# Kernel tuning notes

Hardware: AMD Instinct MI355X
Metric: run time of the kernel (lower is better)

Reference implementation:

```python
import jax, jax.numpy as jnp
import numpy as np

B, S, D, H = 8, 512, 1024, 8
DPH = D // H            # 128, dim per head
MAX_REL = 32
NGRAM = 2               # 2-gram RNN on heads 4..7
NG_START, NG_COUNT = 4, 4
SCALE = float(DPH) ** 0.5


def setup_inputs() -> dict:
    key = jax.random.key(0)
    ks = jax.random.split(key, 12)
    w = lambda k, shp: jax.random.normal(k, shp, jnp.float32) * 0.02
    return {
        "x": jax.random.normal(ks[0], (B, S, D), jnp.float32),
        "mask": jax.random.randint(ks[1], (B, 1, S), 0, 2).astype(bool),
        "Wq": w(ks[2], (D, D)), "bq": jnp.zeros((D,), jnp.float32),
        "Wk": w(ks[3], (D, D)), "bk": jnp.zeros((D,), jnp.float32),
        "Wv": w(ks[4], (D, D)), "bv": jnp.zeros((D,), jnp.float32),
        "Wo": w(ks[5], (D, D)), "bo": jnp.zeros((D,), jnp.float32),
        "rel_emb": w(ks[6], (2 * MAX_REL + 1, DPH)),
        "Wih_f": w(ks[7], (DPH, DPH)), "Whh_f": w(ks[8], (DPH, DPH)),
        "bih_f": jnp.zeros((DPH,), jnp.float32), "bhh_f": jnp.zeros((DPH,), jnp.float32),
        "Wih_b": w(ks[9], (DPH, DPH)), "Whh_b": w(ks[10], (DPH, DPH)),
        "bih_b": jnp.zeros((DPH,), jnp.float32), "bhh_b": jnp.zeros((DPH,), jnp.float32),
    }


def reference(x, mask, Wq, bq, Wk, bk, Wv, bv, Wo, bo, rel_emb,
              Wih_f, Whh_f, bih_f, bhh_f, Wih_b, Whh_b, bih_b, bhh_b):
    shape_h = lambda t: t.reshape(B, S, H, DPH).transpose(0, 2, 1, 3)  # [B,H,S,d]
    q = shape_h(x @ Wq.T + bq)
    k = shape_h(x @ Wk.T + bk)
    v = shape_h(x @ Wv.T + bv)

    # --- ngram path: zero masked positions in q/k/v (all heads) ---
    m = mask[:, :, :, None]  # [B,1,S,1] broadcast over heads and d
    q = jnp.where(m, 0.0, q)
    k = jnp.where(m, 0.0, k)
    v = jnp.where(m, 0.0, v)

    # per-head 2-gram bidirectional RNN on heads NG_START..NG_START+NG_COUNT-1
    qh = q[:, NG_START:NG_START + NG_COUNT].reshape(-1, S, DPH)
    kh = k[:, NG_START:NG_START + NG_COUNT].reshape(-1, S, DPH)
    vh = v[:, NG_START:NG_START + NG_COUNT].reshape(-1, S, DPH)
    feats = jnp.concatenate([qh, kh, vh], axis=0)          # [3*B*NG_COUNT, S, d]
    shifted = jnp.pad(feats, ((0, 0), (1, 0), (0, 0)))[:, :-1]  # shift-by-1 (prev token)
    seq = jnp.stack([shifted, feats], axis=0).reshape(NGRAM, -1, DPH)  # [T, N*S, d]
    h0 = jnp.zeros((seq.shape[1], DPH), jnp.float32)
    fstep = lambda h, xt: (jnp.tanh(xt @ Wih_f.T + bih_f + h @ Whh_f.T + bhh_f), None)
    bstep = lambda h, xt: (jnp.tanh(xt @ Wih_b.T + bih_b + h @ Whh_b.T + bhh_b), None)
    hf, _ = jax.lax.scan(fstep, h0, seq)            # fwd final hidden
    hb, _ = jax.lax.scan(bstep, h0, seq[::-1])      # bwd final hidden
    yy = (hf + hb).reshape(3, B, NG_COUNT, S, DPH)  # sum of direction finals
    q = q.at[:, NG_START:NG_START + NG_COUNT].set(yy[0])
    k = k.at[:, NG_START:NG_START + NG_COUNT].set(yy[1])
    v = v.at[:, NG_START:NG_START + NG_COUNT].set(yy[2])

    # --- relative-position attention ---
    qs = q / SCALE
    r = jnp.arange(S)
    rel_idx = jnp.clip(r[None, :] - r[:, None], -MAX_REL, MAX_REL) + MAX_REL  # [S,S]
    rel_k = rel_emb[rel_idx]  # [S,S,d]; same table used for keys and values
    scores = jnp.einsum('bhqd,bhkd->bhqk', qs, k) + jnp.einsum('bhqd,qkd->bhqk', qs, rel_k)
    scores = jnp.where(mask[:, None], -1e18, scores)  # [B,1,1,S] broadcast
    attn = jax.nn.softmax(scores, axis=-1)
    ctx = jnp.einsum('bhqk,bhkd->bhqd', attn, v) + jnp.einsum('bhqk,qkd->bhqd', attn, rel_k)
    out = ctx.transpose(0, 2, 1, 3).reshape(B, S, D) @ Wo.T + bo
    return out, attn
```

## Files before the change

### kernel.cpp

```cpp
#include <hip/hip_runtime.h>


typedef __bf16 bf16x8 __attribute__((ext_vector_type(8)));
typedef float f32x4 __attribute__((ext_vector_type(4)));

#define MFMA16(a, b, c) __builtin_amdgcn_mfma_f32_16x16x32_bf16(a, b, c, 0, 0, 0)

__device__ __forceinline__ unsigned short f2bf(float f) {
  unsigned u = __float_as_uint(f);
  u += 0x7FFFu + ((u >> 16) & 1u);
  return (unsigned short)(u >> 16);
}
__device__ __forceinline__ uint2 pack4(float4 f) {
  uint2 r;
  r.x = (unsigned)f2bf(f.x) | ((unsigned)f2bf(f.y) << 16);
  r.y = (unsigned)f2bf(f.z) | ((unsigned)f2bf(f.w) << 16);
  return r;
}
__device__ __forceinline__ void gld16(const unsigned short* g, unsigned short* l) {
  __builtin_amdgcn_global_load_lds(
      (const __attribute__((address_space(1))) unsigned int*)g,
      (__attribute__((address_space(3))) unsigned int*)l, 16, 0, 0);
}

__global__ __launch_bounds__(256) void prep_bf16(
    const float* __restrict__ x,
    const float* __restrict__ Wq, const float* __restrict__ Wk,
    const float* __restrict__ Wv, const float* __restrict__ Wo,
    const float* __restrict__ Wihf, const float* __restrict__ Whhf,
    const float* __restrict__ Wihb, const float* __restrict__ Whhb,
    unsigned short* __restrict__ xb, unsigned short* __restrict__ Wqkvb,
    unsigned short* __restrict__ Wob, unsigned short* __restrict__ Wrnnb) {
  int i = blockIdx.x * 256 + threadIdx.x;
  const float* src;
  unsigned short* dst;
  int off;
  if (i < 1048576) {
    src = x; dst = xb; off = i;
  } else if (i < 1310720) {
    src = Wq; dst = Wqkvb; off = i - 1048576;
  } else if (i < 1572864) {
    src = Wk; dst = Wqkvb + 1048576; off = i - 1310720;
  } else if (i < 1835008) {
    src = Wv; dst = Wqkvb + 2097152; off = i - 1572864;
  } else if (i < 2097152) {
    src = Wo; dst = Wob; off = i - 1835008;
  } else if (i < 2101248) {
    src = Wihf; dst = Wrnnb; off = i - 2097152;
  } else if (i < 2105344) {
    src = Whhf; dst = Wrnnb + 16384; off = i - 2101248;
  } else if (i < 2109440) {
    src = Wihb; dst = Wrnnb + 32768; off = i - 2105344;
  } else {
    src = Whhb; dst = Wrnnb + 49152; off = i - 2109440;
  }
  float4 f = *((const float4*)src + off);
  *(uint2*)(dst + (size_t)off * 4) = pack4(f);
}

__global__ __launch_bounds__(256) void qkv_proj(
    const unsigned short* __restrict__ xb, const unsigned short* __restrict__ Wqkvb,
    const float* __restrict__ bq, const float* __restrict__ bk,
    const float* __restrict__ bv, const int* __restrict__ mask,
    unsigned short* __restrict__ qb, unsigned short* __restrict__ kb,
    unsigned short* __restrict__ vb, unsigned short* __restrict__ vT) {
  __shared__ __align__(16) unsigned short As[128 * 64];
  __shared__ __align__(16) unsigned short Bs[128 * 64];
  const int bm = blockIdx.x & 31;
  const int bn = blockIdx.x >> 5;
  const int t = bn >> 3;
  const int nloc0 = (bn & 7) * 128;
  const unsigned short* W = Wqkvb + (size_t)t * 1048576;
  const float* bias = (t == 0) ? bq : (t == 1) ? bk : bv;
  const int tid = threadIdx.x;
  const int lane = tid & 63, w = tid >> 6;
  const int wm = (w >> 1) * 64, wn = (w & 1) * 64;
  const int lanelo = lane & 15, quad = lane >> 4;
  const int row0 = bm * 128;
  const int rloc = lane >> 3, pch = lane & 7;
  const int lch = (pch - rloc) & 7;

  f32x4 acc[4][4];
  const f32x4 zf = {0.f, 0.f, 0.f, 0.f};
#pragma unroll
  for (int i = 0; i < 4; ++i)
#pragma unroll
    for (int j = 0; j < 4; ++j) acc[i][j] = zf;

  for (int kt = 0; kt < 16; ++kt) {
#pragma unroll
    for (int q = 0; q < 4; ++q) {
      int seg = w * 4 + q;
      int grow = seg * 8 + rloc;
      gld16(xb + (size_t)(row0 + grow) * 1024 + kt * 64 + lch * 8, &As[seg * 512]);
      gld16(W + (size_t)(nloc0 + grow) * 1024 + kt * 64 + lch * 8, &Bs[seg * 512]);
    }
    __syncthreads();
#pragma unroll
    for (int ks = 0; ks < 2; ++ks) {
      const int pA = (ks * 4 + quad + lanelo) & 7;
      bf16x8 a[4], bb[4];
#pragma unroll
      for (int i = 0; i < 4; ++i)
        a[i] = *(const bf16x8*)(&As[(wm + i * 16 + lanelo) * 64 + pA * 8]);
#pragma unroll
      for (int j = 0; j < 4; ++j)
        bb[j] = *(const bf16x8*)(&Bs[(wn + j * 16 + lanelo) * 64 + pA * 8]);
#pragma unroll
      for (int i = 0; i < 4; ++i)
#pragma unroll
        for (int j = 0; j < 4; ++j) acc[i][j] = MFMA16(a[i], bb[j], acc[i][j]);
    }
    __syncthreads();
  }
#pragma unroll
  for (int i = 0; i < 4; ++i) {
#pragma unroll
    for (int j = 0; j < 4; ++j) {
      int jj = nloc0 + wn + j * 16 + lanelo;
      int hh = jj >> 7, dc = jj & 127;
      float bvv = bias[jj];
      int m0 = row0 + wm + i * 16 + quad * 4;
      int b0 = m0 >> 9, sS = m0 & 511;
      unsigned short ov[4];
#pragma unroll
      for (int r = 0; r < 4; ++r) {
        int s = sS + r;
        float val = acc[i][j][r] + bvv;
        if (mask[b0 * 512 + s]) val = 0.f;
        unsigned short o = f2bf(val);
        ov[r] = o;
        size_t off = ((size_t)(b0 * 8 + hh) * 512 + s) * 128 + dc;
        if (t == 0) qb[off] = o;
        else if (t == 1) kb[off] = o;
        else vb[off] = o;
      }
      if (t == 2) {
        uint2 pk;
        pk.x = (unsigned)ov[0] | ((unsigned)ov[1] << 16);
        pk.y = (unsigned)ov[2] | ((unsigned)ov[3] << 16);
        *(uint2*)(&vT[((size_t)(b0 * 8 + hh) * 128 + dc) * 512 + sS]) = pk;
      }
    }
  }
}

__global__ __launch_bounds__(256) void prep_rel(
    const float* __restrict__ rel, unsigned short* __restrict__ relb,
    unsigned short* __restrict__ relT) {
  int i = blockIdx.x * 256 + threadIdx.x;
  if (i < 65 * 128) relb[i] = f2bf(rel[i]);
  if (i < 128 * 96) {
    int d = i / 96, r = i - d * 96;
    relT[i] = (r < 65) ? f2bf(rel[r * 128 + d]) : (unsigned short)0;
  }
}

__global__ __launch_bounds__(256) void rnn_fused(
    const unsigned short* __restrict__ qb, const unsigned short* __restrict__ kb,
    const unsigned short* __restrict__ vb,
    const unsigned short* __restrict__ Wrnnb,
    const float* __restrict__ bihf, const float* __restrict__ bhhf,
    const float* __restrict__ bihb, const float* __restrict__ bhhb,
    unsigned short* __restrict__ rnn_out) {
  __shared__ __align__(16) unsigned short X[65 * 136];
  __shared__ __align__(16) unsigned short Wi[128 * 136];
  __shared__ __align__(16) unsigned short Wh[128 * 136];
  __shared__ __align__(16) unsigned short H1[64 * 136];
  __shared__ float cbf[128], cbb[128];

  const unsigned short* Wihfb = Wrnnb;
  const unsigned short* Whhfb = Wrnnb + 16384;
  const unsigned short* Wihbb = Wrnnb + 32768;
  const unsigned short* Whhbb = Wrnnb + 49152;

  const int gid = blockIdx.x;
  const int tile = gid & 7;
  const int g = gid >> 3;
  const int t = g >> 5;
  const int rem = g & 31;
  const int b = rem >> 2, h = (rem & 3) + 4;
  const int s0 = tile * 64;
  const unsigned short* src = (t == 0) ? qb : (t == 1) ? kb : vb;
  const size_t rowbase = (size_t)(b * 8 + h) * 512;
  const int tid = threadIdx.x;

  for (int c = tid; c < 65 * 16; c += 256) {
    int r = c >> 4, cc = c & 15;
    uint4 v4;
    if (r == 0 && s0 == 0) v4 = make_uint4(0, 0, 0, 0);
    else v4 = *(const uint4*)(src + (rowbase + (s0 - 1 + r)) * 128 + cc * 8);
    *(uint4*)(&X[r * 136 + cc * 8]) = v4;
  }
#pragma unroll
  for (int p = 0; p < 8; ++p) {
    int c = p * 256 + tid;
    int r = c >> 4, cc = c & 15;
    *(uint4*)(&Wi[r * 136 + cc * 8]) = *(const uint4*)(Wihfb + c * 8);
    *(uint4*)(&Wh[r * 136 + cc * 8]) = *(const uint4*)(Whhfb + c * 8);
  }
  if (tid < 128) {
    cbf[tid] = bihf[tid] + bhhf[tid];
    cbb[tid] = bihb[tid] + bhhb[tid];
  }
  __syncthreads();

  const int lane = tid & 63, w = tid >> 6;
  const int lanelo = lane & 15, quad = lane >> 4;
  const int marow = w * 16 + lanelo;
  const f32x4 zf = {0.f, 0.f, 0.f, 0.f};

  f32x4 g1[8];
#pragma unroll
  for (int j = 0; j < 8; ++j) g1[j] = zf;
#pragma unroll
  for (int ks = 0; ks < 4; ++ks) {
    bf16x8 a = *(const bf16x8*)(&X[marow * 136 + ks * 32 + quad * 8]);
#pragma unroll
    for (int j = 0; j < 8; ++j) {
      bf16x8 bb = *(const bf16x8*)(&Wi[(j * 16 + lanelo) * 136 + ks * 32 + quad * 8]);
      g1[j] = MFMA16(a, bb, g1[j]);
    }
  }
#pragma unroll
  for (int j = 0; j < 8; ++j) {
    int col = j * 16 + lanelo;
    float cb = cbf[col];
#pragma unroll
    for (int i = 0; i < 4; ++i) {
      int row = w * 16 + quad * 4 + i;
      H1[row * 136 + col] = f2bf(tanhf(g1[j][i] + cb));
    }
  }
  __syncthreads();
  f32x4 a2[8];
#pragma unroll
  for (int j = 0; j < 8; ++j) a2[j] = zf;
#pragma unroll
  for (int ks = 0; ks < 4; ++ks) {
    bf16x8 a = *(const bf16x8*)(&X[(marow + 1) * 136 + ks * 32 + quad * 8]);
#pragma unroll
    for (int j = 0; j < 8; ++j) {
      bf16x8 bb = *(const bf16x8*)(&Wi[(j * 16 + lanelo) * 136 + ks * 32 + quad * 8]);
      a2[j] = MFMA16(a, bb, a2[j]);
    }
  }
#pragma unroll
  for (int ks = 0; ks < 4; ++ks) {
    bf16x8 a = *(const bf16x8*)(&H1[marow * 136 + ks * 32 + quad * 8]);
#pragma unroll
    for (int j = 0; j < 8; ++j) {
      bf16x8 bb = *(const bf16x8*)(&Wh[(j * 16 + lanelo) * 136 + ks * 32 + quad * 8]);
      a2[j] = MFMA16(a, bb, a2[j]);
    }
  }
  float outF[8][4];
#pragma unroll
  for (int j = 0; j < 8; ++j) {
    int col = j * 16 + lanelo;
    float cb = cbf[col];
#pragma unroll
    for (int i = 0; i < 4; ++i) outF[j][i] = tanhf(a2[j][i] + cb);
  }
  __syncthreads();
#pragma unroll
  for (int p = 0; p < 8; ++p) {
    int c = p * 256 + tid;
    int r = c >> 4, cc = c & 15;
    *(uint4*)(&Wi[r * 136 + cc * 8]) = *(const uint4*)(Wihbb + c * 8);
    *(uint4*)(&Wh[r * 136 + cc * 8]) = *(const uint4*)(Whhbb + c * 8);
  }
  __syncthreads();
#pragma unroll
  for (int j = 0; j < 8; ++j) g1[j] = zf;
#pragma unroll
  for (int ks = 0; ks < 4; ++ks) {
    bf16x8 a = *(const bf16x8*)(&X[(marow + 1) * 136 + ks * 32 + quad * 8]);
#pragma unroll
    for (int j = 0; j < 8; ++j) {
      bf16x8 bb = *(const bf16x8*)(&Wi[(j * 16 + lanelo) * 136 + ks * 32 + quad * 8]);
      g1[j] = MFMA16(a, bb, g1[j]);
    }
  }
#pragma unroll
  for (int j = 0; j < 8; ++j) {
    int col = j * 16 + lanelo;
    float cb = cbb[col];
#pragma unroll
    for (int i = 0; i < 4; ++i) {
      int row = w * 16 + quad * 4 + i;
      H1[row * 136 + col] = f2bf(tanhf(g1[j][i] + cb));
    }
  }
  __syncthreads();
#pragma unroll
  for (int j = 0; j < 8; ++j) a2[j] = zf;
#pragma unroll
  for (int ks = 0; ks < 4; ++ks) {
    bf16x8 a = *(const bf16x8*)(&X[marow * 136 + ks * 32 + quad * 8]);
#pragma unroll
    for (int j = 0; j < 8; ++j) {
      bf16x8 bb = *(const bf16x8*)(&Wi[(j * 16 + lanelo) * 136 + ks * 32 + quad * 8]);
      a2[j] = MFMA16(a, bb, a2[j]);
    }
  }
#pragma unroll
  for (int ks = 0; ks < 4; ++ks) {
    bf16x8 a = *(const bf16x8*)(&H1[marow * 136 + ks * 32 + quad * 8]);
#pragma unroll
    for (int j = 0; j < 8; ++j) {
      bf16x8 bb = *(const bf16x8*)(&Wh[(j * 16 + lanelo) * 136 + ks * 32 + quad * 8]);
      a2[j] = MFMA16(a, bb, a2[j]);
    }
  }
#pragma unroll
  for (int j = 0; j < 8; ++j) {
    int col = j * 16 + lanelo;
    float cb = cbb[col];
#pragma unroll
    for (int i = 0; i < 4; ++i) {
      int row = w * 16 + quad * 4 + i;
      float val = outF[j][i] + tanhf(a2[j][i] + cb);
      rnn_out[((size_t)g * 512 + s0 + row) * 128 + col] = f2bf(val);
    }
  }
}

__global__ __launch_bounds__(256) void rnn_copyback(
    const unsigned short* __restrict__ rnn_out,
    unsigned short* __restrict__ qb, unsigned short* __restrict__ kb,
    unsigned short* __restrict__ vT) {
  int idx = blockIdx.x * 256 + threadIdx.x;
  int g = idx >> 16;
  int r2 = idx & 65535;
  int s = r2 >> 7, col = r2 & 127;
  int t = g >> 5, rem = g & 31, b = rem >> 2, h = (rem & 3) + 4;
  unsigned short val = rnn_out[idx];
  size_t off = ((size_t)(b * 8 + h) * 512 + s) * 128 + col;
  if (t == 0) qb[off] = val;
  else if (t == 1) kb[off] = val;
  else vT[((size_t)(b * 8 + h) * 128 + col) * 512 + s] = val;
}

__global__ __launch_bounds__(256) void scores_softmax(
    const unsigned short* __restrict__ qbuf, const unsigned short* __restrict__ kbuf,
    const unsigned short* __restrict__ relb, const int* __restrict__ mask,
    float* __restrict__ attn_out, unsigned short* __restrict__ abuf) {
  __shared__ __align__(16) unsigned short As[64 * 136];
  __shared__ __align__(16) unsigned short Bs[512 * 32];
  __shared__ float Ps[64 * 80];
  __shared__ float cmask[512];
  const int idx = blockIdx.x;
  const int qt = idx & 7, bh = idx >> 3, b = bh >> 3;
  const int q0 = qt * 64;
  const size_t qrow0 = (size_t)bh * 512 + q0;
  const int tid = threadIdx.x;

  for (int i = tid; i < 64 * 96; i += 256) abuf[qrow0 * 96 + i] = 0;
  for (int c = tid; c < 1024; c += 256) {
    int r = c >> 4, cc = c & 15;
    *(uint4*)(&As[r * 136 + cc * 8]) = *(const uint4*)(qbuf + (qrow0 + r) * 128 + cc * 8);
  }
  for (int i = tid; i < 512; i += 256) cmask[i] = mask[b * 512 + i] ? -1e9f : 0.f;
  __syncthreads();

  const int lane = tid & 63, w = tid >> 6;
  const int lanelo = lane & 15, quad = lane >> 4;
  const int rloc4 = lane >> 2, pch4 = lane & 3;
  const int lch4 = (pch4 - rloc4) & 3;
  const int pB = (quad + lanelo) & 3;
  const f32x4 zf = {0.f, 0.f, 0.f, 0.f};

  f32x4 pacc[5];
#pragma unroll
  for (int j = 0; j < 5; ++j) pacc[j] = zf;
  for (int ks = 0; ks < 4; ++ks) {
    for (int c = tid; c < 320; c += 256) {
      int r = c >> 2, cc = c & 3;
      uint4 v4 = (r < 65) ? *(const uint4*)(relb + r * 128 + ks * 32 + cc * 8)
                          : make_uint4(0, 0, 0, 0);
      *(uint4*)(&Bs[r * 32 + ((cc + r) & 3) * 8]) = v4;
    }
    __syncthreads();
    bf16x8 a = *(const bf16x8*)(&As[(w * 16 + lanelo) * 136 + ks * 32 + quad * 8]);
#pragma unroll
    for (int j = 0; j < 5; ++j) {
      bf16x8 bb = *(const bf16x8*)(&Bs[(j * 16 + lanelo) * 32 + pB * 8]);
      pacc[j] = MFMA16(a, bb, pacc[j]);
    }
    __syncthreads();
  }
#pragma unroll
  for (int j = 0; j < 5; ++j) {
    int col = j * 16 + lanelo;
#pragma unroll
    for (int i = 0; i < 4; ++i) Ps[(w * 16 + quad * 4 + i) * 80 + col] = pacc[j][i];
  }
  __syncthreads();

  f32x4 acc[32];
#pragma unroll
  for (int j = 0; j < 32; ++j) acc[j] = zf;
  for (int ks = 0; ks < 4; ++ks) {
#pragma unroll
    for (int q = 0; q < 8; ++q) {
      int seg = w * 8 + q;
      int grow = seg * 16 + rloc4;
      gld16(kbuf + ((size_t)bh * 512 + grow) * 128 + ks * 32 + lch4 * 8,
            &Bs[seg * 512]);
    }
    __syncthreads();
    bf16x8 a = *(const bf16x8*)(&As[(w * 16 + lanelo) * 136 + ks * 32 + quad * 8]);
#pragma unroll
    for (int j = 0; j < 32; ++j) {
      bf16x8 bb = *(const bf16x8*)(&Bs[(j * 16 + lanelo) * 32 + pB * 8]);
      acc[j] = MFMA16(a, bb, acc[j]);
    }
    __syncthreads();
  }

  const float rscale = 0.08838834764831845f;
  float mrow[4] = {-1.0e30f, -1.0e30f, -1.0e30f, -1.0e30f};
#pragma unroll
  for (int j = 0; j < 32; ++j) {
    int k = j * 16 + lanelo;
    float cm = cmask[k];
#pragma unroll
    for (int i = 0; i < 4; ++i) {
      int row = w * 16 + quad * 4 + i;
      int qg = q0 + row;
      int d = k - qg;
      int r = min(max(d, -32), 32) + 32;
      float val = (acc[j][i] + Ps[row * 80 + r]) * rscale + cm;
      acc[j][i] = val;
      mrow[i] = fmaxf(mrow[i], val);
    }
  }
#pragma unroll
  for (int st = 1; st < 16; st <<= 1)
#pragma unroll
    for (int i = 0; i < 4; ++i) mrow[i] = fmaxf(mrow[i], __shfl_xor(mrow[i], st, 64));
  float srow[4] = {0.f, 0.f, 0.f, 0.f};
#pragma unroll
  for (int j = 0; j < 32; ++j)
#pragma unroll
    for (int i = 0; i < 4; ++i) {
      float e = __expf(acc[j][i] - mrow[i]);
      acc[j][i] = e;
      srow[i] += e;
    }
#pragma unroll
  for (int st = 1; st < 16; st <<= 1)
#pragma unroll
    for (int i = 0; i < 4; ++i) srow[i] += __shfl_xor(srow[i], st, 64);
  float rs[4];
#pragma unroll
  for (int i = 0; i < 4; ++i) rs[i] = (srow[i] > 0.f) ? 1.f / srow[i] : 0.f;

  float s0a[4] = {0.f, 0.f, 0.f, 0.f}, s64a[4] = {0.f, 0.f, 0.f, 0.f};
#pragma unroll
  for (int j = 0; j < 32; ++j) {
    int k = j * 16 + lanelo;
#pragma unroll
    for (int i = 0; i < 4; ++i) {
      int row = w * 16 + quad * 4 + i;
      int qg = q0 + row;
      float at = acc[j][i] * rs[i];
      attn_out[((size_t)bh * 512 + qg) * 512 + k] = at;
      int d = k - qg;
      if (d <= -32) s0a[i] += at;
      else if (d >= 32) s64a[i] += at;
      else abuf[((size_t)bh * 512 + qg) * 96 + (d + 32)] = f2bf(at);
    }
  }
#pragma unroll
  for (int st = 1; st < 16; st <<= 1)
#pragma unroll
    for (int i = 0; i < 4; ++i) {
      s0a[i] += __shfl_xor(s0a[i], st, 64);
      s64a[i] += __shfl_xor(s64a[i], st, 64);
    }
  if (lanelo == 0) {
#pragma unroll
    for (int i = 0; i < 4; ++i) {
      int qg = q0 + w * 16 + quad * 4 + i;
      abuf[((size_t)bh * 512 + qg) * 96 + 0] = f2bf(s0a[i]);
      abuf[((size_t)bh * 512 + qg) * 96 + 64] = f2bf(s64a[i]);
    }
  }
}

__global__ __launch_bounds__(256) void av_ctx(
    const float* __restrict__ attn, const unsigned short* __restrict__ abuf,
    const unsigned short* __restrict__ vT, const unsigned short* __restrict__ relT,
    unsigned short* __restrict__ ctx) {
  __shared__ __align__(16) unsigned short As[64 * 40];
  __shared__ __align__(16) unsigned short Bs[128 * 32];
  const int idx = blockIdx.x;
  const int qt = idx & 7, bh = idx >> 3;
  const int q0 = qt * 64;
  const int tid = threadIdx.x, lane = tid & 63, w = tid >> 6;
  const int lanelo = lane & 15, quad = lane >> 4;
  const int rloc4 = lane >> 2, pch4 = lane & 3;
  const int lch4 = (pch4 - rloc4) & 3;
  const int pB = (quad + lanelo) & 3;
  const f32x4 zf = {0.f, 0.f, 0.f, 0.f};
  f32x4 acc[8];
#pragma unroll
  for (int j = 0; j < 8; ++j) acc[j] = zf;

  for (int kt = 0; kt < 19; ++kt) {
    {
      int c = tid;
      int r = c >> 2, cc = c & 3;
      if (kt < 16) {
        const float* src = attn + ((size_t)bh * 512 + q0 + r) * 512 + kt * 32 + cc * 8;
        *(uint2*)(&As[r * 40 + cc * 8]) = pack4(*(const float4*)(src));
        *(uint2*)(&As[r * 40 + cc * 8 + 4]) = pack4(*(const float4*)(src + 4));
      } else {
        *(uint4*)(&As[r * 40 + cc * 8]) =
            *(const uint4*)(abuf + ((size_t)bh * 512 + q0 + r) * 96 + (kt - 16) * 32 + cc * 8);
      }
    }
#pragma unroll
    for (int q = 0; q < 2; ++q) {
      int seg = w * 2 + q;
      int grow = seg * 16 + rloc4;
      if (kt < 16)
        gld16(vT + ((size_t)bh * 128 + grow) * 512 + kt * 32 + lch4 * 8, &Bs[seg * 512]);
      else
        gld16(relT + grow * 96 + (kt - 16) * 32 + lch4 * 8, &Bs[seg * 512]);
    }
    __syncthreads();
    bf16x8 a = *(const bf16x8*)(&As[(w * 16 + lanelo) * 40 + quad * 8]);
#pragma unroll
    for (int j = 0; j < 8; ++j) {
      bf16x8 bb = *(const bf16x8*)(&Bs[(j * 16 + lanelo) * 32 + pB * 8]);
      acc[j] = MFMA16(a, bb, acc[j]);
    }
    __syncthreads();
  }
  const int b = bh >> 3, h = bh & 7;
#pragma unroll
  for (int j = 0; j < 8; ++j) {
    int d = j * 16 + lanelo;
#pragma unroll
    for (int i = 0; i < 4; ++i) {
      int qg = q0 + w * 16 + quad * 4 + i;
      ctx[((size_t)(b * 512 + qg)) * 1024 + h * 128 + d] = f2bf(acc[j][i]);
    }
  }
}

__global__ __launch_bounds__(256) void out_proj(
    const unsigned short* __restrict__ ctx, const unsigned short* __restrict__ Wob,
    const float* __restrict__ bo, float* __restrict__ outp) {
  __shared__ __align__(16) unsigned short As[128 * 64];
  __shared__ __align__(16) unsigned short Bs[128 * 64];
  const int bm = blockIdx.x & 31, bn = blockIdx.x >> 5;
  const int tid = threadIdx.x, lane = tid & 63, w = tid >> 6;
  const int wm = (w >> 1) * 64, wn = (w & 1) * 64;
  const int lanelo = lane & 15, quad = lane >> 4;
  const int row0 = bm * 128, col0 = bn * 128;
  const int rloc = lane >> 3, pch = lane & 7;
  const int lch = (pch - rloc) & 7;
  f32x4 acc[4][4];
  const f32x4 zf = {0.f, 0.f, 0.f, 0.f};
#pragma unroll
  for (int i = 0; i < 4; ++i)
#pragma unroll
    for (int j = 0; j < 4; ++j) acc[i][j] = zf;

  for (int kt = 0; kt < 16; ++kt) {
#pragma unroll
    for (int q = 0; q < 4; ++q) {
      int seg = w * 4 + q;
      int grow = seg * 8 + rloc;
      gld16(ctx + (size_t)(row0 + grow) * 1024 + kt * 64 + lch * 8, &As[seg * 512]);
      gld16(Wob + (size_t)(col0 + grow) * 1024 + kt * 64 + lch * 8, &Bs[seg * 512]);
    }
    __syncthreads();
#pragma unroll
    for (int ks = 0; ks < 2; ++ks) {
      const int pA = (ks * 4 + quad + lanelo) & 7;
      bf16x8 a[4], bb[4];
#pragma unroll
      for (int i = 0; i < 4; ++i)
        a[i] = *(const bf16x8*)(&As[(wm + i * 16 + lanelo) * 64 + pA * 8]);
#pragma unroll
      for (int j = 0; j < 4; ++j)
        bb[j] = *(const bf16x8*)(&Bs[(wn + j * 16 + lanelo) * 64 + pA * 8]);
#pragma unroll
      for (int i = 0; i < 4; ++i)
#pragma unroll
        for (int j = 0; j < 4; ++j) acc[i][j] = MFMA16(a[i], bb[j], acc[i][j]);
    }
    __syncthreads();
  }
#pragma unroll
  for (int i = 0; i < 4; ++i) {
#pragma unroll
    for (int j = 0; j < 4; ++j) {
      int n = col0 + wn + j * 16 + lanelo;
      float bbv = bo[n];
#pragma unroll
      for (int r = 0; r < 4; ++r) {
        int m = row0 + wm + i * 16 + quad * 4 + r;
        outp[(size_t)m * 1024 + n] = acc[i][j][r] + bbv;
      }
    }
  }
}

extern "C" void kernel_launch(void* const* d_in, const int* in_sizes, int n_in,
                              void* d_out, int out_size, void* d_ws, size_t ws_size,
                              hipStream_t stream) {
  const float* x    = (const float*)d_in[0];
  const int*   mask = (const int*)d_in[1];
  const float* Wq   = (const float*)d_in[2];
  const float* bq   = (const float*)d_in[3];
  const float* Wk   = (const float*)d_in[4];
  const float* bk   = (const float*)d_in[5];
  const float* Wv   = (const float*)d_in[6];
  const float* bv   = (const float*)d_in[7];
  const float* Wo   = (const float*)d_in[8];
  const float* bo   = (const float*)d_in[9];
  const float* rel  = (const float*)d_in[10];
  const float* Wihf = (const float*)d_in[11];
  const float* Whhf = (const float*)d_in[12];
  const float* bihf = (const float*)d_in[13];
  const float* bhhf = (const float*)d_in[14];
  const float* Wihb = (const float*)d_in[15];
  const float* Whhb = (const float*)d_in[16];
  const float* bihb = (const float*)d_in[17];
  const float* bhhb = (const float*)d_in[18];

  char* ws = (char*)d_ws;
  unsigned short* qb   = (unsigned short*)(ws + 0);
  unsigned short* kb   = (unsigned short*)(ws + 8388608);
  unsigned short* vT   = (unsigned short*)(ws + 16777216);
  unsigned short* abuf = (unsigned short*)(ws + 25165824);
  unsigned short* relb = (unsigned short*)(ws + 31457280);
  unsigned short* relT = (unsigned short*)(ws + 31473920);
  unsigned short* Wob  = (unsigned short*)(ws + 31498496);
  unsigned short* ctx  = qb;

  float* outp  = (float*)d_out;
  float* attnF = outp + 4194304;
  unsigned short* abase  = (unsigned short*)attnF;
  unsigned short* xb     = abase;
  unsigned short* vb     = abase + 4194304;
  unsigned short* rnnout = abase + 8388608;
  unsigned short* Wqkvb  = abase + 14680064;
  unsigned short* Wrnnb  = abase + 17825792;

  prep_bf16<<<dim3(8256), dim3(256), 0, stream>>>(
      x, Wq, Wk, Wv, Wo, Wihf, Whhf, Wihb, Whhb, xb, Wqkvb, Wob, Wrnnb);
  prep_rel<<<dim3(48), dim3(256), 0, stream>>>(rel, relb, relT);
  qkv_proj<<<dim3(768), dim3(256), 0, stream>>>(xb, Wqkvb, bq, bk, bv, mask,
                                                qb, kb, vb, vT);
  rnn_fused<<<dim3(768), dim3(256), 0, stream>>>(qb, kb, vb, Wrnnb,
                                                 bihf, bhhf, bihb, bhhb, rnnout);
  rnn_copyback<<<dim3(24576), dim3(256), 0, stream>>>(rnnout, qb, kb, vT);
  scores_softmax<<<dim3(512), dim3(256), 0, stream>>>(qb, kb, relb, mask, attnF, abuf);
  av_ctx<<<dim3(512), dim3(256), 0, stream>>>(attnF, abuf, vT, relT, ctx);
  out_proj<<<dim3(256), dim3(256), 0, stream>>>(ctx, Wob, bo, outp);
}
```

Measured before the change: 356.7 us.

## Fuse scores/softmax with attention-value product and convert Wo inside out_proj

```diff
diff --git a/kernel.cpp b/kernel.cpp
--- a/kernel.cpp
+++ b/kernel.cpp
@@ -26,11 +26,11 @@
 __global__ __launch_bounds__(256) void prep_bf16(
     const float* __restrict__ x,
     const float* __restrict__ Wq, const float* __restrict__ Wk,
-    const float* __restrict__ Wv, const float* __restrict__ Wo,
+    const float* __restrict__ Wv,
     const float* __restrict__ Wihf, const float* __restrict__ Whhf,
     const float* __restrict__ Wihb, const float* __restrict__ Whhb,
     unsigned short* __restrict__ xb, unsigned short* __restrict__ Wqkvb,
-    unsigned short* __restrict__ Wob, unsigned short* __restrict__ Wrnnb) {
+    unsigned short* __restrict__ Wrnnb) {
   int i = blockIdx.x * 256 + threadIdx.x;
   const float* src;
   unsigned short* dst;
@@ -43,16 +43,14 @@
     src = Wk; dst = Wqkvb + 1048576; off = i - 1310720;
   } else if (i < 1835008) {
     src = Wv; dst = Wqkvb + 2097152; off = i - 1572864;
-  } else if (i < 2097152) {
-    src = Wo; dst = Wob; off = i - 1835008;
-  } else if (i < 2101248) {
-    src = Wihf; dst = Wrnnb; off = i - 2097152;
-  } else if (i < 2105344) {
-    src = Whhf; dst = Wrnnb + 16384; off = i - 2101248;
-  } else if (i < 2109440) {
-    src = Wihb; dst = Wrnnb + 32768; off = i - 2105344;
+  } else if (i < 1839104) {
+    src = Wihf; dst = Wrnnb; off = i - 1835008;
+  } else if (i < 1843200) {
+    src = Whhf; dst = Wrnnb + 16384; off = i - 1839104;
+  } else if (i < 1847296) {
+    src = Wihb; dst = Wrnnb + 32768; off = i - 1843200;
   } else {
-    src = Whhb; dst = Wrnnb + 49152; off = i - 2109440;
+    src = Whhb; dst = Wrnnb + 49152; off = i - 1847296;
   }
   float4 f = *((const float4*)src + off);
   *(uint2*)(dst + (size_t)off * 4) = pack4(f);
@@ -342,34 +340,41 @@
   else vT[((size_t)(b * 8 + h) * 128 + col) * 512 + s] = val;
 }
 
-__global__ __launch_bounds__(256) void scores_softmax(
+__global__ __launch_bounds__(256, 2) void scores_av_fused(
     const unsigned short* __restrict__ qbuf, const unsigned short* __restrict__ kbuf,
-    const unsigned short* __restrict__ relb, const int* __restrict__ mask,
-    float* __restrict__ attn_out, unsigned short* __restrict__ abuf) {
-  __shared__ __align__(16) unsigned short As[64 * 136];
-  __shared__ __align__(16) unsigned short Bs[512 * 32];
-  __shared__ float Ps[64 * 80];
-  __shared__ float cmask[512];
+    const unsigned short* __restrict__ relb, const unsigned short* __restrict__ vT,
+    const unsigned short* __restrict__ relT, const float* __restrict__ relf,
+    const int* __restrict__ mask, float* __restrict__ attn_out,
+    unsigned short* __restrict__ ctx) {
+  __shared__ __align__(16) char smem[81920];
+  unsigned short* As = (unsigned short*)smem;
+  unsigned short* Bs = (unsigned short*)(smem + 17408);
+  float* Ps = (float*)(smem + 50176);
+  float* cmaskS = (float*)(smem + 71680);
+  unsigned short* abufT = (unsigned short*)(smem + 73728);
+  unsigned short* attnb = (unsigned short*)smem;
+  unsigned short* Bs2 = (unsigned short*)(smem + 65536);
+  float* redb = (float*)(smem + 65536);
+
   const int idx = blockIdx.x;
   const int qt = idx & 7, bh = idx >> 3, b = bh >> 3;
   const int q0 = qt * 64;
   const size_t qrow0 = (size_t)bh * 512 + q0;
   const int tid = threadIdx.x;
-
-  for (int i = tid; i < 64 * 96; i += 256) abuf[qrow0 * 96 + i] = 0;
-  for (int c = tid; c < 1024; c += 256) {
-    int r = c >> 4, cc = c & 15;
-    *(uint4*)(&As[r * 136 + cc * 8]) = *(const uint4*)(qbuf + (qrow0 + r) * 128 + cc * 8);
-  }
-  for (int i = tid; i < 512; i += 256) cmask[i] = mask[b * 512 + i] ? -1e9f : 0.f;
-  __syncthreads();
-
   const int lane = tid & 63, w = tid >> 6;
   const int lanelo = lane & 15, quad = lane >> 4;
   const int rloc4 = lane >> 2, pch4 = lane & 3;
   const int lch4 = (pch4 - rloc4) & 3;
   const int pB = (quad + lanelo) & 3;
   const f32x4 zf = {0.f, 0.f, 0.f, 0.f};
+
+  for (int c = tid; c < 1024; c += 256) {
+    int r = c >> 4, cc = c & 15;
+    *(uint4*)(&As[r * 136 + cc * 8]) = *(const uint4*)(qbuf + (qrow0 + r) * 128 + cc * 8);
+  }
+  for (int i = tid; i < 512; i += 256) cmaskS[i] = mask[b * 512 + i] ? -1e9f : 0.f;
+  for (int i = tid; i < 512; i += 256) *(uint4*)(&abufT[i * 8]) = make_uint4(0, 0, 0, 0);
+  __syncthreads();
 
   f32x4 pacc[5];
 #pragma unroll
@@ -382,178 +387,239 @@
       *(uint4*)(&Bs[r * 32 + ((cc + r) & 3) * 8]) = v4;
     }
     __syncthreads();
-    bf16x8 a = *(const bf16x8*)(&As[(w * 16 + lanelo) * 136 + ks * 32 + quad * 8]);
+    bf16x8 qf_ = *(const bf16x8*)(&As[(w * 16 + lanelo) * 136 + ks * 32 + quad * 8]);
 #pragma unroll
     for (int j = 0; j < 5; ++j) {
-      bf16x8 bb = *(const bf16x8*)(&Bs[(j * 16 + lanelo) * 32 + pB * 8]);
-      pacc[j] = MFMA16(a, bb, pacc[j]);
-    }
-    __syncthreads();
-  }
-#pragma unroll
-  for (int j = 0; j < 5; ++j) {
-    int col = j * 16 + lanelo;
-#pragma unroll
-    for (int i = 0; i < 4; ++i) Ps[(w * 16 + quad * 4 + i) * 80 + col] = pacc[j][i];
-  }
-  __syncthreads();
-
-  f32x4 acc[32];
-#pragma unroll
-  for (int j = 0; j < 32; ++j) acc[j] = zf;
+      bf16x8 rf_ = *(const bf16x8*)(&Bs[(j * 16 + lanelo) * 32 + pB * 8]);
+      pacc[j] = MFMA16(rf_, qf_, pacc[j]);
+    }
+    __syncthreads();
+  }
+#pragma unroll
+  for (int j = 0; j < 5; ++j)
+    *(f32x4*)(&Ps[(w * 16 + lanelo) * 84 + j * 16 + quad * 4]) = pacc[j];
+
+  f32x4 acc[8][4];
+#pragma unroll
+  for (int kf = 0; kf < 8; ++kf)
+#pragma unroll
+    for (int nf = 0; nf < 4; ++nf) acc[kf][nf] = zf;
   for (int ks = 0; ks < 4; ++ks) {
 #pragma unroll
-    for (int q = 0; q < 8; ++q) {
-      int seg = w * 8 + q;
+    for (int qq = 0; qq < 8; ++qq) {
+      int seg = w * 8 + qq;
       int grow = seg * 16 + rloc4;
       gld16(kbuf + ((size_t)bh * 512 + grow) * 128 + ks * 32 + lch4 * 8,
             &Bs[seg * 512]);
     }
     __syncthreads();
-    bf16x8 a = *(const bf16x8*)(&As[(w * 16 + lanelo) * 136 + ks * 32 + quad * 8]);
-#pragma unroll
-    for (int j = 0; j < 32; ++j) {
-      bf16x8 bb = *(const bf16x8*)(&Bs[(j * 16 + lanelo) * 32 + pB * 8]);
-      acc[j] = MFMA16(a, bb, acc[j]);
+    bf16x8 qfr[4];
+#pragma unroll
+    for (int nf = 0; nf < 4; ++nf)
+      qfr[nf] = *(const bf16x8*)(&As[(nf * 16 + lanelo) * 136 + ks * 32 + quad * 8]);
+#pragma unroll
+    for (int kf = 0; kf < 8; ++kf) {
+      bf16x8 kfr = *(const bf16x8*)(&Bs[((w * 8 + kf) * 16 + lanelo) * 32 + pB * 8]);
+#pragma unroll
+      for (int nf = 0; nf < 4; ++nf) acc[kf][nf] = MFMA16(kfr, qfr[nf], acc[kf][nf]);
     }
     __syncthreads();
   }
 
   const float rscale = 0.08838834764831845f;
-  float mrow[4] = {-1.0e30f, -1.0e30f, -1.0e30f, -1.0e30f};
-#pragma unroll
-  for (int j = 0; j < 32; ++j) {
-    int k = j * 16 + lanelo;
-    float cm = cmask[k];
-#pragma unroll
-    for (int i = 0; i < 4; ++i) {
-      int row = w * 16 + quad * 4 + i;
-      int qg = q0 + row;
-      int d = k - qg;
-      int r = min(max(d, -32), 32) + 32;
-      float val = (acc[j][i] + Ps[row * 80 + r]) * rscale + cm;
-      acc[j][i] = val;
-      mrow[i] = fmaxf(mrow[i], val);
-    }
-  }
-#pragma unroll
-  for (int st = 1; st < 16; st <<= 1)
-#pragma unroll
-    for (int i = 0; i < 4; ++i) mrow[i] = fmaxf(mrow[i], __shfl_xor(mrow[i], st, 64));
-  float srow[4] = {0.f, 0.f, 0.f, 0.f};
-#pragma unroll
-  for (int j = 0; j < 32; ++j)
-#pragma unroll
-    for (int i = 0; i < 4; ++i) {
-      float e = __expf(acc[j][i] - mrow[i]);
-      acc[j][i] = e;
-      srow[i] += e;
-    }
-#pragma unroll
-  for (int st = 1; st < 16; st <<= 1)
-#pragma unroll
-    for (int i = 0; i < 4; ++i) srow[i] += __shfl_xor(srow[i], st, 64);
+  float pmax[4] = {-3e38f, -3e38f, -3e38f, -3e38f};
+#pragma unroll
+  for (int qf = 0; qf < 4; ++qf) {
+    const int q = qf * 16 + lanelo;
+    const int qg = q0 + q;
+    const float* PsR = &Ps[q * 84];
+#pragma unroll
+    for (int kf = 0; kf < 8; ++kf) {
+      const int kbase = w * 128 + kf * 16 + quad * 4;
+#pragma unroll
+      for (int i = 0; i < 4; ++i) {
+        int k = kbase + i;
+        int d = k - qg;
+        int r = min(max(d, -32), 32) + 32;
+        float val = (acc[kf][qf][i] + PsR[r]) * rscale + cmaskS[k];
+        acc[kf][qf][i] = val;
+        pmax[qf] = fmaxf(pmax[qf], val);
+      }
+    }
+  }
+  float* red_max = redb;
+  float* red_sum = redb + 256;
+  float* red_s0 = redb + 512;
+  float* red_s64 = redb + 768;
+#pragma unroll
+  for (int qf = 0; qf < 4; ++qf) {
+    pmax[qf] = fmaxf(pmax[qf], __shfl_xor(pmax[qf], 16, 64));
+    pmax[qf] = fmaxf(pmax[qf], __shfl_xor(pmax[qf], 32, 64));
+  }
+  if (quad == 0) {
+#pragma unroll
+    for (int qf = 0; qf < 4; ++qf) red_max[w * 64 + qf * 16 + lanelo] = pmax[qf];
+  }
+  __syncthreads();
+  float mf_[4], psum[4];
+#pragma unroll
+  for (int qf = 0; qf < 4; ++qf) {
+    int q = qf * 16 + lanelo;
+    mf_[qf] = fmaxf(fmaxf(red_max[q], red_max[64 + q]),
+                    fmaxf(red_max[128 + q], red_max[192 + q]));
+    psum[qf] = 0.f;
+  }
+#pragma unroll
+  for (int qf = 0; qf < 4; ++qf)
+#pragma unroll
+    for (int kf = 0; kf < 8; ++kf)
+#pragma unroll
+      for (int i = 0; i < 4; ++i) {
+        float e = __expf(acc[kf][qf][i] - mf_[qf]);
+        acc[kf][qf][i] = e;
+        psum[qf] += e;
+      }
+#pragma unroll
+  for (int qf = 0; qf < 4; ++qf) {
+    psum[qf] += __shfl_xor(psum[qf], 16, 64);
+    psum[qf] += __shfl_xor(psum[qf], 32, 64);
+  }
+  if (quad == 0) {
+#pragma unroll
+    for (int qf = 0; qf < 4; ++qf) red_sum[w * 64 + qf * 16 + lanelo] = psum[qf];
+  }
+  __syncthreads();
   float rs[4];
 #pragma unroll
-  for (int i = 0; i < 4; ++i) rs[i] = (srow[i] > 0.f) ? 1.f / srow[i] : 0.f;
-
-  float s0a[4] = {0.f, 0.f, 0.f, 0.f}, s64a[4] = {0.f, 0.f, 0.f, 0.f};
-#pragma unroll
-  for (int j = 0; j < 32; ++j) {
-    int k = j * 16 + lanelo;
-#pragma unroll
-    for (int i = 0; i < 4; ++i) {
-      int row = w * 16 + quad * 4 + i;
-      int qg = q0 + row;
-      float at = acc[j][i] * rs[i];
-      attn_out[((size_t)bh * 512 + qg) * 512 + k] = at;
-      int d = k - qg;
-      if (d <= -32) s0a[i] += at;
-      else if (d >= 32) s64a[i] += at;
-      else abuf[((size_t)bh * 512 + qg) * 96 + (d + 32)] = f2bf(at);
-    }
-  }
-#pragma unroll
-  for (int st = 1; st < 16; st <<= 1)
-#pragma unroll
-    for (int i = 0; i < 4; ++i) {
-      s0a[i] += __shfl_xor(s0a[i], st, 64);
-      s64a[i] += __shfl_xor(s64a[i], st, 64);
-    }
-  if (lanelo == 0) {
-#pragma unroll
-    for (int i = 0; i < 4; ++i) {
-      int qg = q0 + w * 16 + quad * 4 + i;
-      abuf[((size_t)bh * 512 + qg) * 96 + 0] = f2bf(s0a[i]);
-      abuf[((size_t)bh * 512 + qg) * 96 + 64] = f2bf(s64a[i]);
-    }
-  }
-}
-
-__global__ __launch_bounds__(256) void av_ctx(
-    const float* __restrict__ attn, const unsigned short* __restrict__ abuf,
-    const unsigned short* __restrict__ vT, const unsigned short* __restrict__ relT,
-    unsigned short* __restrict__ ctx) {
-  __shared__ __align__(16) unsigned short As[64 * 40];
-  __shared__ __align__(16) unsigned short Bs[128 * 32];
-  const int idx = blockIdx.x;
-  const int qt = idx & 7, bh = idx >> 3;
-  const int q0 = qt * 64;
-  const int tid = threadIdx.x, lane = tid & 63, w = tid >> 6;
-  const int lanelo = lane & 15, quad = lane >> 4;
-  const int rloc4 = lane >> 2, pch4 = lane & 3;
-  const int lch4 = (pch4 - rloc4) & 3;
-  const int pB = (quad + lanelo) & 3;
-  const f32x4 zf = {0.f, 0.f, 0.f, 0.f};
-  f32x4 acc[8];
-#pragma unroll
-  for (int j = 0; j < 8; ++j) acc[j] = zf;
-
-  for (int kt = 0; kt < 19; ++kt) {
-    {
-      int c = tid;
-      int r = c >> 2, cc = c & 3;
-      if (kt < 16) {
-        const float* src = attn + ((size_t)bh * 512 + q0 + r) * 512 + kt * 32 + cc * 8;
-        *(uint2*)(&As[r * 40 + cc * 8]) = pack4(*(const float4*)(src));
-        *(uint2*)(&As[r * 40 + cc * 8 + 4]) = pack4(*(const float4*)(src + 4));
-      } else {
-        *(uint4*)(&As[r * 40 + cc * 8]) =
-            *(const uint4*)(abuf + ((size_t)bh * 512 + q0 + r) * 96 + (kt - 16) * 32 + cc * 8);
-      }
-    }
-#pragma unroll
-    for (int q = 0; q < 2; ++q) {
-      int seg = w * 2 + q;
+  for (int qf = 0; qf < 4; ++qf) {
+    int q = qf * 16 + lanelo;
+    float s = red_sum[q] + red_sum[64 + q] + red_sum[128 + q] + red_sum[192 + q];
+    rs[qf] = (s > 0.f) ? 1.f / s : 0.f;
+  }
+
+  float s0p[4] = {0.f, 0.f, 0.f, 0.f}, s64p[4] = {0.f, 0.f, 0.f, 0.f};
+#pragma unroll
+  for (int qf = 0; qf < 4; ++qf) {
+    const int q = qf * 16 + lanelo;
+    const int qg = q0 + q;
+#pragma unroll
+    for (int kf = 0; kf < 8; ++kf) {
+      const int kbase = w * 128 + kf * 16 + quad * 4;
+      float4 at;
+      float* ap = (float*)&at;
+#pragma unroll
+      for (int i = 0; i < 4; ++i) {
+        float v = acc[kf][qf][i] * rs[qf];
+        ap[i] = v;
+        int d = kbase + i - qg;
+        if (d <= -32) s0p[qf] += v;
+        else if (d >= 32) s64p[qf] += v;
+        else {
+          int col = d + 32;
+          abufT[q * 64 + (((col >> 3) + q) & 7) * 8 + (col & 7)] = f2bf(v);
+        }
+      }
+      *(float4*)(&attn_out[((size_t)bh * 512 + qg) * 512 + kbase]) = at;
+      uint2 pk = pack4(at);
+      int cc = kbase >> 3;
+      *(uint2*)(&attnb[q * 512 + ((cc + q) & 63) * 8 + (quad & 1) * 4]) = pk;
+    }
+  }
+#pragma unroll
+  for (int qf = 0; qf < 4; ++qf) {
+    s0p[qf] += __shfl_xor(s0p[qf], 16, 64);
+    s0p[qf] += __shfl_xor(s0p[qf], 32, 64);
+    s64p[qf] += __shfl_xor(s64p[qf], 16, 64);
+    s64p[qf] += __shfl_xor(s64p[qf], 32, 64);
+  }
+  if (quad == 0) {
+#pragma unroll
+    for (int qf = 0; qf < 4; ++qf) {
+      red_s0[w * 64 + qf * 16 + lanelo] = s0p[qf];
+      red_s64[w * 64 + qf * 16 + lanelo] = s64p[qf];
+    }
+  }
+  __syncthreads();
+  float s0f[4], s64f[4];
+#pragma unroll
+  for (int qf = 0; qf < 4; ++qf) {
+    int q = qf * 16 + lanelo;
+    s0f[qf] = red_s0[q] + red_s0[64 + q] + red_s0[128 + q] + red_s0[192 + q];
+    s64f[qf] = red_s64[q] + red_s64[64 + q] + red_s64[128 + q] + red_s64[192 + q];
+  }
+  __syncthreads();
+
+  f32x4 cacc[2][4];
+#pragma unroll
+  for (int mf = 0; mf < 2; ++mf)
+#pragma unroll
+    for (int nf = 0; nf < 4; ++nf) cacc[mf][nf] = zf;
+  for (int kt = 0; kt < 18; ++kt) {
+#pragma unroll
+    for (int qq = 0; qq < 2; ++qq) {
+      int seg = w * 2 + qq;
       int grow = seg * 16 + rloc4;
       if (kt < 16)
-        gld16(vT + ((size_t)bh * 128 + grow) * 512 + kt * 32 + lch4 * 8, &Bs[seg * 512]);
+        gld16(vT + ((size_t)bh * 128 + grow) * 512 + kt * 32 + lch4 * 8, &Bs2[seg * 512]);
       else
-        gld16(relT + grow * 96 + (kt - 16) * 32 + lch4 * 8, &Bs[seg * 512]);
-    }
-    __syncthreads();
-    bf16x8 a = *(const bf16x8*)(&As[(w * 16 + lanelo) * 40 + quad * 8]);
-#pragma unroll
-    for (int j = 0; j < 8; ++j) {
-      bf16x8 bb = *(const bf16x8*)(&Bs[(j * 16 + lanelo) * 32 + pB * 8]);
-      acc[j] = MFMA16(a, bb, acc[j]);
-    }
-    __syncthreads();
-  }
-  const int b = bh >> 3, h = bh & 7;
-#pragma unroll
-  for (int j = 0; j < 8; ++j) {
-    int d = j * 16 + lanelo;
+        gld16(relT + grow * 96 + (kt - 16) * 32 + lch4 * 8, &Bs2[seg * 512]);
+    }
+    __syncthreads();
+    bf16x8 afr[2], bfr[4];
+#pragma unroll
+    for (int mf = 0; mf < 2; ++mf)
+      afr[mf] = *(const bf16x8*)(&Bs2[((w * 2 + mf) * 16 + lanelo) * 32 + pB * 8]);
+    if (kt < 16) {
+#pragma unroll
+      for (int nf = 0; nf < 4; ++nf) {
+        int q = nf * 16 + lanelo;
+        bfr[nf] = *(const bf16x8*)(&attnb[q * 512 + ((kt * 4 + quad + q) & 63) * 8]);
+      }
+    } else {
+#pragma unroll
+      for (int nf = 0; nf < 4; ++nf) {
+        int q = nf * 16 + lanelo;
+        bfr[nf] = *(const bf16x8*)(&abufT[q * 64 + (((kt - 16) * 4 + quad + q) & 7) * 8]);
+      }
+    }
+#pragma unroll
+    for (int mf = 0; mf < 2; ++mf)
+#pragma unroll
+      for (int nf = 0; nf < 4; ++nf) cacc[mf][nf] = MFMA16(afr[mf], bfr[nf], cacc[mf][nf]);
+    __syncthreads();
+  }
+
+  float r0v[2][4], r64v[2][4];
+#pragma unroll
+  for (int mf = 0; mf < 2; ++mf)
 #pragma unroll
     for (int i = 0; i < 4; ++i) {
-      int qg = q0 + w * 16 + quad * 4 + i;
-      ctx[((size_t)(b * 512 + qg)) * 1024 + h * 128 + d] = f2bf(acc[j][i]);
+      int d = w * 32 + mf * 16 + quad * 4 + i;
+      r0v[mf][i] = relf[d];
+      r64v[mf][i] = relf[64 * 128 + d];
+    }
+  const int b_ = bh >> 3, h_ = bh & 7;
+#pragma unroll
+  for (int nf = 0; nf < 4; ++nf) {
+    int qg = q0 + nf * 16 + lanelo;
+#pragma unroll
+    for (int mf = 0; mf < 2; ++mf) {
+      unsigned short ov[4];
+#pragma unroll
+      for (int i = 0; i < 4; ++i) {
+        float val = cacc[mf][nf][i] + s0f[nf] * r0v[mf][i] + s64f[nf] * r64v[mf][i];
+        ov[i] = f2bf(val);
+      }
+      uint2 pk;
+      pk.x = (unsigned)ov[0] | ((unsigned)ov[1] << 16);
+      pk.y = (unsigned)ov[2] | ((unsigned)ov[3] << 16);
+      *(uint2*)(&ctx[((size_t)(b_ * 512 + qg)) * 1024 + h_ * 128 + w * 32 + mf * 16 + quad * 4]) = pk;
     }
   }
 }
 
 __global__ __launch_bounds__(256) void out_proj(
-    const unsigned short* __restrict__ ctx, const unsigned short* __restrict__ Wob,
+    const unsigned short* __restrict__ ctx, const float* __restrict__ Wo,
     const float* __restrict__ bo, float* __restrict__ outp) {
   __shared__ __align__(16) unsigned short As[128 * 64];
   __shared__ __align__(16) unsigned short Bs[128 * 64];
@@ -577,7 +643,13 @@
       int seg = w * 4 + q;
       int grow = seg * 8 + rloc;
       gld16(ctx + (size_t)(row0 + grow) * 1024 + kt * 64 + lch * 8, &As[seg * 512]);
-      gld16(Wob + (size_t)(col0 + grow) * 1024 + kt * 64 + lch * 8, &Bs[seg * 512]);
+    }
+    for (int c = tid; c < 1024; c += 256) {
+      int r = c >> 3, cc2 = c & 7;
+      const float* src = Wo + (size_t)(col0 + r) * 1024 + kt * 64 + cc2 * 8;
+      int pc = (cc2 + r) & 7;
+      *(uint2*)(&Bs[r * 64 + pc * 8]) = pack4(*(const float4*)src);
+      *(uint2*)(&Bs[r * 64 + pc * 8 + 4]) = pack4(*(const float4*)(src + 4));
     }
     __syncthreads();
 #pragma unroll
@@ -639,11 +711,9 @@
   unsigned short* qb   = (unsigned short*)(ws + 0);
   unsigned short* kb   = (unsigned short*)(ws + 8388608);
   unsigned short* vT   = (unsigned short*)(ws + 16777216);
-  unsigned short* abuf = (unsigned short*)(ws + 25165824);
-  unsigned short* relb = (unsigned short*)(ws + 31457280);
-  unsigned short* relT = (unsigned short*)(ws + 31473920);
-  unsigned short* Wob  = (unsigned short*)(ws + 31498496);
-  unsigned short* ctx  = qb;
+  unsigned short* ctx  = (unsigned short*)(ws + 25165824);
+  unsigned short* relb = (unsigned short*)(ws + 33554432);
+  unsigned short* relT = (unsigned short*)(ws + 33571072);
 
   float* outp  = (float*)d_out;
   float* attnF = outp + 4194304;
@@ -654,15 +724,15 @@
   unsigned short* Wqkvb  = abase + 14680064;
   unsigned short* Wrnnb  = abase + 17825792;
 
-  prep_bf16<<<dim3(8256), dim3(256), 0, stream>>>(
-      x, Wq, Wk, Wv, Wo, Wihf, Whhf, Wihb, Whhb, xb, Wqkvb, Wob, Wrnnb);
+  prep_bf16<<<dim3(7232), dim3(256), 0, stream>>>(
+      x, Wq, Wk, Wv, Wihf, Whhf, Wihb, Whhb, xb, Wqkvb, Wrnnb);
   prep_rel<<<dim3(48), dim3(256), 0, stream>>>(rel, relb, relT);
   qkv_proj<<<dim3(768), dim3(256), 0, stream>>>(xb, Wqkvb, bq, bk, bv, mask,
                                                 qb, kb, vb, vT);
   rnn_fused<<<dim3(768), dim3(256), 0, stream>>>(qb, kb, vb, Wrnnb,
                                                  bihf, bhhf, bihb, bhhb, rnnout);
   rnn_copyback<<<dim3(24576), dim3(256), 0, stream>>>(rnnout, qb, kb, vT);
-  scores_softmax<<<dim3(512), dim3(256), 0, stream>>>(qb, kb, relb, mask, attnF, abuf);
-  av_ctx<<<dim3(512), dim3(256), 0, stream>>>(attnF, abuf, vT, relT, ctx);
-  out_proj<<<dim3(256), dim3(256), 0, stream>>>(ctx, Wob, bo, outp);
-}
+  scores_av_fused<<<dim3(512), dim3(256), 0, stream>>>(qb, kb, relb, vT, relT,
+                                                       rel, mask, attnF, ctx);
+  out_proj<<<dim3(256), dim3(256), 0, stream>>>(ctx, Wo, bo, outp);
+}
```

Measured after the change: 532.4 us. +49.3%, slower.
